# Performance work log

Measured on AMD Instinct MI355X. Metric: run time of the kernel, lower is better.

## Reference

```python
import jax, jax.numpy as jnp
import numpy as np

B, S, D, H = 2, 2048, 2048, 16
DEPTH = D // H


def setup_inputs() -> dict:
    key = jax.random.key(0)
    ks = jax.random.split(key, 12)
    std = 1.0 / np.sqrt(D)
    mk = lambda k, shape: (jax.random.uniform(k, shape, jnp.float32) * 2 - 1) * std
    # causal additive mask: 1.0 where future position (masked), 0.0 elsewhere
    mask = jnp.triu(jnp.ones((S, S), jnp.float32), k=1)[None, None]
    return {
        "q": jax.random.normal(ks[0], (B, S, D), jnp.float32),
        "k": jax.random.normal(ks[1], (B, S, D), jnp.float32),
        "v": jax.random.normal(ks[2], (B, S, D), jnp.float32),
        "mask": mask,
        "wq_w": mk(ks[3], (D, D)), "wq_b": mk(ks[4], (D,)),
        "wk_w": mk(ks[5], (D, D)), "wk_b": mk(ks[6], (D,)),
        "wv_w": mk(ks[7], (D, D)), "wv_b": mk(ks[8], (D,)),
        "dense_w": mk(ks[9], (D, D)), "dense_b": mk(ks[10], (D,)),
    }


def split_heads(x):
    # [B,S,D] -> [B,H,S,depth]
    b, s, _ = x.shape
    return x.reshape(b, s, H, DEPTH).transpose(0, 2, 1, 3)


def reference(q, k, v, mask, wq_w, wq_b, wk_w, wk_b, wv_w, wv_b, dense_w, dense_b):
    # torch Linear: y = x @ W.T + b
    qh = split_heads(q @ wq_w.T + wq_b)
    kh = split_heads(k @ wk_w.T + wk_b)
    vh = split_heads(v @ wv_w.T + wv_b)
    scale = 1.0 / jnp.sqrt(jnp.asarray(DEPTH, jnp.float32))
    logits = jnp.einsum("bhqd,bhkd->bhqk", qh, kh) * scale
    logits = logits + mask * (-1e9)
    weights = jax.nn.softmax(logits, axis=-1)  # dropout is identity in eval
    out = jnp.einsum("bhqk,bhkd->bhqd", weights, vh)
    out = out.transpose(0, 2, 1, 3).reshape(q.shape[0], -1, D)
    return out @ dense_w.T + dense_b
```

## Files before the change

### kernel.cpp

```cpp
#include <hip/hip_runtime.h>
#include <hip/hip_bf16.h>


typedef __bf16 bf16x8 __attribute__((ext_vector_type(8)));
typedef float f32x4 __attribute__((ext_vector_type(4)));
typedef float f32x16 __attribute__((ext_vector_type(16)));
typedef unsigned short u16;
typedef unsigned int u32;

#define DEV static __device__ __forceinline__

DEV void gload_lds16(const void* g, void* l) {
  __builtin_amdgcn_global_load_lds(
      (const __attribute__((address_space(1))) void*)g,
      (__attribute__((address_space(3))) void*)l, 16, 0, 0);
}

DEV f32x4 mfma16(bf16x8 a, bf16x8 b, f32x4 c) {
  return __builtin_amdgcn_mfma_f32_16x16x32_bf16(a, b, c, 0, 0, 0);
}

DEV f32x16 mfma32(bf16x8 a, bf16x8 b, f32x16 c) {
  return __builtin_amdgcn_mfma_f32_32x32x16_bf16(a, b, c, 0, 0, 0);
}

DEV u16 f2bf(float x) {
  return __builtin_bit_cast(u16, __float2bfloat16(x));
}

DEV u32 pack2(float lo, float hi_) {
  return (u32)f2bf(lo) | ((u32)f2bf(hi_) << 16);
}

__global__ void __launch_bounds__(256) conv_f32_bf16(
    const float* __restrict__ in, u16* __restrict__ out) {
  const size_t i = ((size_t)blockIdx.x * 256 + threadIdx.x) * 4;
  const float4 v = *reinterpret_cast<const float4*>(in + i);
  ushort4 o;
  o.x = f2bf(v.x); o.y = f2bf(v.y); o.z = f2bf(v.z); o.w = f2bf(v.w);
  *reinterpret_cast<ushort4*>(out + i) = o;
}

__global__ void __launch_bounds__(256) conv_all(
    const float* __restrict__ s0, const float* __restrict__ s1,
    const float* __restrict__ s2, const float* __restrict__ s3,
    const float* __restrict__ s4, const float* __restrict__ s5,
    const float* __restrict__ s6,
    u16* __restrict__ d0, u16* __restrict__ d1, u16* __restrict__ d2,
    u16* __restrict__ d3, u16* __restrict__ d4, u16* __restrict__ d5,
    u16* __restrict__ d6, const size_t nact, const size_t nw) {
  const int j = blockIdx.y;
  const size_t i = ((size_t)blockIdx.x * 256 + threadIdx.x) * 4;
  const float* s; u16* d; size_t n;
  switch (j) {
    case 0: s = s0; d = d0; n = nact; break;
    case 1: s = s1; d = d1; n = nact; break;
    case 2: s = s2; d = d2; n = nact; break;
    case 3: s = s3; d = d3; n = nw; break;
    case 4: s = s4; d = d4; n = nw; break;
    case 5: s = s5; d = d5; n = nw; break;
    default: s = s6; d = d6; n = nw; break;
  }
  if (i >= n) return;
  const float4 v = *reinterpret_cast<const float4*>(s + i);
  ushort4 o;
  o.x = f2bf(v.x); o.y = f2bf(v.y); o.z = f2bf(v.z); o.w = f2bf(v.w);
  *reinterpret_cast<ushort4*>(d + i) = o;
}

#define GBM 128
#define GBN 128
#define GBK 32
#define GK 2048
#define GNT 64

DEV void gemm_core(const u16* __restrict__ A, const u16* __restrict__ Bw,
                   const float* __restrict__ bias, void* __restrict__ Cout,
                   const int m0, const int n0, const int N, const int out_f32,
                   u16* As, u16* Bs) {
  const int tid = threadIdx.x;
  const int lane = tid & 63;
  const int w = tid >> 6;
  const int wr = w >> 1, wc = w & 1;
  const int g = lane >> 4;
  const int r16 = lane & 15;

  int offA[2], offB[2], dst2[2];
#pragma unroll
  for (int rr = 0; rr < 2; ++rr) {
    const int G = rr * 64 + lane;
    const int rp = w * 16 + (G >> 3);
    const int s = (G & 7) ^ (rp & 7);
    const int row = rp * 2 + (s >> 2);
    const int ch = s & 3;
    offA[rr] = (m0 + row) * GK + ch * 8;
    offB[rr] = (n0 + row) * GK + ch * 8;
    dst2[rr] = w * 1024 + rr * 512;
  }

  f32x4 acc[4][4];
#pragma unroll
  for (int i = 0; i < 4; ++i)
#pragma unroll
    for (int j = 0; j < 4; ++j) acc[i][j] = {0.f, 0.f, 0.f, 0.f};

  auto stage = [&](int t) {
    const int kk = t * GBK;
    u16* as = As + (t & 3) * 4096;
    u16* bs = Bs + (t & 3) * 4096;
    gload_lds16(A + offA[0] + kk, as + dst2[0]);
    gload_lds16(A + offA[1] + kk, as + dst2[1]);
    gload_lds16(Bw + offB[0] + kk, bs + dst2[0]);
    gload_lds16(Bw + offB[1] + kk, bs + dst2[1]);
  };

  auto compute = [&](int t) {
    const u16* as = As + (t & 3) * 4096;
    const u16* bs = Bs + (t & 3) * 4096;
    bf16x8 af[4], bf[4];
#pragma unroll
    for (int i = 0; i < 4; ++i) {
      const int row = wr * 64 + i * 16 + r16;
      const int rp = row >> 1;
      const int sl = (((row & 1) << 2) | g) ^ (rp & 7);
      af[i] = *reinterpret_cast<const bf16x8*>(as + rp * 64 + sl * 8);
      const int rowb = wc * 64 + i * 16 + r16;
      const int rpb = rowb >> 1;
      const int slb = (((rowb & 1) << 2) | g) ^ (rpb & 7);
      bf[i] = *reinterpret_cast<const bf16x8*>(bs + rpb * 64 + slb * 8);
    }
#pragma unroll
    for (int i = 0; i < 4; ++i)
#pragma unroll
      for (int j = 0; j < 4; ++j)
        acc[i][j] = mfma16(af[i], bf[j], acc[i][j]);
  };

  stage(0); stage(1); stage(2);
  asm volatile("s_waitcnt vmcnt(8)" ::: "memory");
  __builtin_amdgcn_s_barrier();

  for (int t = 0; t <= GNT - 4; ++t) {
    stage(t + 3);
    compute(t);
    asm volatile("s_waitcnt vmcnt(8) lgkmcnt(0)" ::: "memory");
    __builtin_amdgcn_s_barrier();
  }
  compute(GNT - 3);
  asm volatile("s_waitcnt vmcnt(4) lgkmcnt(0)" ::: "memory");
  __builtin_amdgcn_s_barrier();
  compute(GNT - 2);
  asm volatile("s_waitcnt vmcnt(0) lgkmcnt(0)" ::: "memory");
  __builtin_amdgcn_s_barrier();
  compute(GNT - 1);

  const int cbase = n0 + wc * 64 + r16;
  const int rbase = m0 + wr * 64 + g * 4;
#pragma unroll
  for (int i = 0; i < 4; ++i) {
#pragma unroll
    for (int j = 0; j < 4; ++j) {
      const int c = cbase + j * 16;
      const float bv = bias[c];
#pragma unroll
      for (int r = 0; r < 4; ++r) {
        const float v = acc[i][j][r] + bv;
        const size_t idx = (size_t)(rbase + i * 16 + r) * N + c;
        if (out_f32) ((float*)Cout)[idx] = v;
        else ((u16*)Cout)[idx] = f2bf(v);
      }
    }
  }
}

__global__ void __launch_bounds__(256, 2) gemm_ring(
    const u16* __restrict__ A, const u16* __restrict__ Bw,
    const float* __restrict__ bias, void* __restrict__ Cout,
    const int Mblocks, const int N, const int out_f32) {
  __shared__ u16 As[4 * GBM * GBK];
  __shared__ u16 Bs[4 * GBN * GBK];
  const int cpx = gridDim.x >> 3;
  int bid = blockIdx.x;
  bid = (bid & 7) * cpx + (bid >> 3);
  const int m0 = (bid % Mblocks) * GBM;
  const int n0 = (bid / Mblocks) * GBN;
  gemm_core(A, Bw, bias, Cout, m0, n0, N, out_f32, As, Bs);
}

__global__ void __launch_bounds__(256, 2) gemm_qkv(
    const u16* __restrict__ A0, const u16* __restrict__ A1,
    const u16* __restrict__ A2, const u16* __restrict__ W0,
    const u16* __restrict__ W1, const u16* __restrict__ W2,
    const float* __restrict__ b0, const float* __restrict__ b1,
    const float* __restrict__ b2, u16* __restrict__ C0,
    u16* __restrict__ C1, u16* __restrict__ C2) {
  __shared__ u16 As[4 * GBM * GBK];
  __shared__ u16 Bs[4 * GBN * GBK];
  const int which = blockIdx.x >> 9;
  const int inner = blockIdx.x & 511;
  const int bid = (inner & 7) * 64 + (inner >> 3);
  const int m0 = (bid & 31) * GBM;
  const int n0 = (bid >> 5) * GBN;
  const u16* A = which == 0 ? A0 : which == 1 ? A1 : A2;
  const u16* W = which == 0 ? W0 : which == 1 ? W1 : W2;
  const float* bb = which == 0 ? b0 : which == 1 ? b1 : b2;
  u16* C = which == 0 ? C0 : which == 1 ? C1 : C2;
  gemm_core(A, W, bb, C, m0, n0, 2048, 0, As, Bs);
}

#define SEQ 2048
#define DMODEL 2048
#define DH 128
#define QBLK 128
#define KBLK 64
#define C1 0.12751744f
#define THR_RAW 62.73f

__global__ void __launch_bounds__(256, 2) flash_attn(
    const u16* __restrict__ Qh, const u16* __restrict__ Kh,
    const u16* __restrict__ Vh, u16* __restrict__ O) {
  __shared__ u16 Ks[KBLK * DH];
  __shared__ u16 Vt[DH * KBLK];

  const int tid = threadIdx.x;
  const int lane = tid & 63;
  const int w = tid >> 6;
  const int hi = lane >> 5;
  const int l31 = lane & 31;

  const int cc = blockIdx.x;
  const int low = cc & 15;
  const int bh = (cc >> 4) & 31;
  const int h = bh & 15;
  const int b = bh >> 4;
  const int g0 = low ^ h;
  const int qt = b ? (15 - g0) : g0;
  const int q0 = qt * QBLK;
  const size_t rowbase = (size_t)b * SEQ;
  const int hoff = h * DH;
  const int qw = q0 + w * 32;
  const int qlane = qw + l31;

  bf16x8 aq[8];
  {
    const u16* qp = &Qh[(rowbase + qlane) * DMODEL + hoff + hi * 8];
#pragma unroll
    for (int c = 0; c < 8; ++c)
      aq[c] = *reinterpret_cast<const bf16x8*>(qp + c * 16);
  }

  f32x16 oacc[4];
#pragma unroll
  for (int dt = 0; dt < 4; ++dt)
#pragma unroll
    for (int r = 0; r < 16; ++r) oacc[dt][r] = 0.f;
  float mrow = -1e30f, lrow = 0.f;

  const int krl = w * 16 + (lane >> 4);
  const int kg4 = w * 4 + (lane >> 4);
  const int du = lane & 15;

  const int nkt = 2 * qt + 2;
  const int ktd = qw >> 6;

  uint4 vv[4];
#pragma unroll
  for (int r = 0; r < 4; ++r)
    vv[r] = *reinterpret_cast<const uint4*>(
        &Vh[(rowbase + kg4 * 4 + r) * DMODEL + hoff + du * 8]);

  for (int kt = 0; kt < nkt; ++kt) {
    const int k0 = kt * KBLK;
    __syncthreads();

#pragma unroll
    for (int i = 0; i < 4; ++i) {
      const int r = krl + i * 4;
      const int cg = (lane & 15) ^ (r & 15);
      gload_lds16(&Kh[(rowbase + k0 + r) * DMODEL + hoff + cg * 8],
                  &Ks[(w * 16 + i * 4) * DH]);
    }

#pragma unroll
    for (int j = 0; j < 8; ++j) {
      const int d = du * 8 + j;
      ushort4 pk4;
      pk4.x = ((const u16*)&vv[0])[j];
      pk4.y = ((const u16*)&vv[1])[j];
      pk4.z = ((const u16*)&vv[2])[j];
      pk4.w = ((const u16*)&vv[3])[j];
      const int slot = (((kg4 >> 1) ^ ((d >> 2) & 7)) * 8) + (kg4 & 1) * 4;
      *reinterpret_cast<ushort4*>(&Vt[d * KBLK + slot]) = pk4;
    }

    __syncthreads();

    if (kt + 1 < nkt) {
#pragma unroll
      for (int r = 0; r < 4; ++r)
        vv[r] = *reinterpret_cast<const uint4*>(
            &Vh[(rowbase + k0 + KBLK + kg4 * 4 + r) * DMODEL + hoff + du * 8]);
    }

    if (kt > ktd) continue;

    const bool diag = (kt == ktd);
    const bool act1 = (kt < ktd) || (w & 1);
    const bool m0q = diag && !(w & 1);
    const bool m1q = diag && (w & 1);

    float p[2][16];
    {
      f32x16 s;
#pragma unroll
      for (int r = 0; r < 16; ++r) s[r] = 0.f;
      __builtin_amdgcn_s_setprio(1);
#pragma unroll
      for (int c = 0; c < 8; ++c) {
        const int row = l31;
        const bf16x8 kf = *reinterpret_cast<const bf16x8*>(
            &Ks[row * DH + (((c * 2 + hi) ^ (row & 15)) * 8)]);
        s = mfma32(kf, aq[c], s);
      }
      __builtin_amdgcn_s_setprio(0);
#pragma unroll
      for (int r = 0; r < 16; ++r) {
        const int krow = (r & 3) + 8 * (r >> 2) + 4 * hi;
        p[0][r] = (m0q && (k0 + krow > qlane)) ? -1e9f : s[r];
      }
    }
    if (act1) {
      f32x16 s;
#pragma unroll
      for (int r = 0; r < 16; ++r) s[r] = 0.f;
      __builtin_amdgcn_s_setprio(1);
#pragma unroll
      for (int c = 0; c < 8; ++c) {
        const int row = 32 + l31;
        const bf16x8 kf = *reinterpret_cast<const bf16x8*>(
            &Ks[row * DH + (((c * 2 + hi) ^ (row & 15)) * 8)]);
        s = mfma32(kf, aq[c], s);
      }
      __builtin_amdgcn_s_setprio(0);
#pragma unroll
      for (int r = 0; r < 16; ++r) {
        const int krow = (r & 3) + 8 * (r >> 2) + 4 * hi;
        p[1][r] = (m1q && (k0 + 32 + krow > qlane)) ? -1e9f : s[r];
      }
    } else {
#pragma unroll
      for (int r = 0; r < 16; ++r) p[1][r] = -1e9f;
    }

    float mx = fmaxf(p[0][0], p[0][1]);
#pragma unroll
    for (int r = 2; r < 16; ++r) mx = fmaxf(mx, p[0][r]);
#pragma unroll
    for (int r = 0; r < 16; ++r) mx = fmaxf(mx, p[1][r]);
    mx = fmaxf(mx, __shfl_xor(mx, 32));

    const bool need = (mx > mrow + THR_RAW);
    if (__any((int)need)) {
      const float mn = fmaxf(mrow, mx);
      const float al = exp2f((mrow - mn) * C1);
      mrow = mn;
      lrow *= al;
#pragma unroll
      for (int r = 0; r < 16; ++r) {
        const float ar = __shfl(al, (r & 3) + 8 * (r >> 2) + 4 * hi);
#pragma unroll
        for (int dt = 0; dt < 4; ++dt) oacc[dt][r] *= ar;
      }
    }

    float sum = 0.f;
#pragma unroll
    for (int t = 0; t < 2; ++t)
#pragma unroll
      for (int r = 0; r < 16; ++r) {
        p[t][r] = exp2f((p[t][r] - mrow) * C1);
        sum += p[t][r];
      }
    sum += __shfl_xor(sum, 32);
    lrow += sum;

    u32 pk[2][8];
#pragma unroll
    for (int t = 0; t < 2; ++t)
#pragma unroll
      for (int m = 0; m < 8; ++m)
        pk[t][m] = pack2(p[t][2 * m], p[t][2 * m + 1]);

    __builtin_amdgcn_s_setprio(1);
#pragma unroll
    for (int ks = 0; ks < 4; ++ks) {
      if (ks >= 2 && !act1) break;
      const int t = ks >> 1;
      const int bs = (ks & 1) * 4;
      const u32 s0 = __shfl_xor(pk[t][bs + 0], 32);
      const u32 s1 = __shfl_xor(pk[t][bs + 1], 32);
      const u32 s2 = __shfl_xor(pk[t][bs + 2], 32);
      const u32 s3 = __shfl_xor(pk[t][bs + 3], 32);
      union { u32 u[4]; bf16x8 v; } pa;
      pa.u[0] = hi ? s2 : pk[t][bs + 0];
      pa.u[1] = hi ? s3 : pk[t][bs + 1];
      pa.u[2] = hi ? pk[t][bs + 2] : s0;
      pa.u[3] = hi ? pk[t][bs + 3] : s1;
#pragma unroll
      for (int dt = 0; dt < 4; ++dt) {
        const int d = dt * 32 + l31;
        const bf16x8 vf = *reinterpret_cast<const bf16x8*>(
            &Vt[d * KBLK + (((ks * 2 + hi) ^ ((d >> 2) & 7)) * 8)]);
        oacc[dt] = mfma32(pa.v, vf, oacc[dt]);
      }
    }
    __builtin_amdgcn_s_setprio(0);
  }

  const float li = __builtin_amdgcn_rcpf(lrow);
#pragma unroll
  for (int r = 0; r < 16; ++r) {
    const int rowq = (r & 3) + 8 * (r >> 2) + 4 * hi;
    const float lr = __shfl(li, rowq);
    u16* op = &O[(rowbase + qw + rowq) * DMODEL + hoff + l31];
#pragma unroll
    for (int dt = 0; dt < 4; ++dt) op[dt * 32] = f2bf(oacc[dt][r] * lr);
  }
}

extern "C" void kernel_launch(void* const* d_in, const int* in_sizes, int n_in,
                              void* d_out, int out_size, void* d_ws,
                              size_t ws_size, hipStream_t stream) {
  const int Bv = 2, S = 2048, D = 2048;
  const int M = Bv * S;
  const size_t NT = (size_t)M * D;
  const size_t NW = (size_t)D * D;

  const float* q = (const float*)d_in[0];
  const float* k = (const float*)d_in[1];
  const float* v = (const float*)d_in[2];
  const float* wq_w = (const float*)d_in[4];
  const float* wq_b = (const float*)d_in[5];
  const float* wk_w = (const float*)d_in[6];
  const float* wk_b = (const float*)d_in[7];
  const float* wv_w = (const float*)d_in[8];
  const float* wv_b = (const float*)d_in[9];
  const float* dw = (const float*)d_in[10];
  const float* db = (const float*)d_in[11];
  float* out = (float*)d_out;

  const dim3 blk(256);
  const dim3 gattn(512);
  const size_t need = (7 * NT + 4 * NW) * 2;

  if (ws_size >= need) {
    u16* base = (u16*)d_ws;
    u16* Xq = base;
    u16* Xk = Xq + NT;
    u16* Xv = Xk + NT;
    u16* Wq = Xv + NT;
    u16* Wk = Wq + NW;
    u16* Wv = Wk + NW;
    u16* Wd = Wv + NW;
    u16* Qh = Wd + NW;
    u16* Kh = Qh + NT;
    u16* Vh = Kh + NT;
    u16* Obf = Vh + NT;

    conv_all<<<dim3((unsigned)(NT / 1024), 7), blk, 0, stream>>>(
        q, k, v, wq_w, wk_w, wv_w, dw, Xq, Xk, Xv, Wq, Wk, Wv, Wd, NT, NW);
    gemm_qkv<<<dim3(1536), blk, 0, stream>>>(
        Xq, Xk, Xv, Wq, Wk, Wv, wq_b, wk_b, wv_b, Qh, Kh, Vh);
    flash_attn<<<gattn, blk, 0, stream>>>(Qh, Kh, Vh, Obf);
    gemm_ring<<<dim3(512), blk, 0, stream>>>(Obf, Wd, db, out, 32, D, 1);
  } else {
    u16* Xbf = (u16*)d_ws;
    u16* Wbf = Xbf + NT;
    u16* Qh = Wbf + NW;
    u16* Kh = Qh + NT;
    u16* Vh = Kh + NT;
    u16* Obf = Vh + NT;
    const dim3 gact((unsigned)(NT / 1024));
    const dim3 gw((unsigned)(NW / 1024));

    conv_f32_bf16<<<gact, blk, 0, stream>>>(q, Xbf);
    conv_f32_bf16<<<gw, blk, 0, stream>>>(wq_w, Wbf);
    gemm_ring<<<dim3(512), blk, 0, stream>>>(Xbf, Wbf, wq_b, Qh, 32, D, 0);
    conv_f32_bf16<<<gact, blk, 0, stream>>>(k, Xbf);
    conv_f32_bf16<<<gw, blk, 0, stream>>>(wk_w, Wbf);
    gemm_ring<<<dim3(512), blk, 0, stream>>>(Xbf, Wbf, wk_b, Kh, 32, D, 0);
    conv_f32_bf16<<<gact, blk, 0, stream>>>(v, Xbf);
    conv_f32_bf16<<<gw, blk, 0, stream>>>(wv_w, Wbf);
    gemm_ring<<<dim3(512), blk, 0, stream>>>(Xbf, Wbf, wv_b, Vh, 32, D, 0);
    flash_attn<<<gattn, blk, 0, stream>>>(Qh, Kh, Vh, Obf);
    conv_f32_bf16<<<gw, blk, 0, stream>>>(dw, Wbf);
    gemm_ring<<<dim3(512), blk, 0, stream>>>(Obf, Wbf, db, out, 32, D, 1);
  }
}
```

Measured before the change: 342.8 us.

## Use 2-wave GEMM blocks with 64x128 warp tiles and 3-stage LDS ring

The GEMM blocks drop from 4 waves to 2 waves, each computing a 64x128 tile with 32 accumulators instead of 16. This raises MFMA work per LDS fragment load. The LDS ring shrinks from 4 to 3 stages, and the QKV launch now interleaves blocks across XCDs with a new block-index mapping. The cost is higher register pressure, fewer waves to hide latency, and a shallower prefetch pipeline.

```diff
diff --git a/kernel.cpp b/kernel.cpp
--- a/kernel.cpp
+++ b/kernel.cpp
@@ -81,86 +81,84 @@
   const int tid = threadIdx.x;
   const int lane = tid & 63;
   const int w = tid >> 6;
-  const int wr = w >> 1, wc = w & 1;
   const int g = lane >> 4;
   const int r16 = lane & 15;
 
-  int offA[2], offB[2], dst2[2];
-#pragma unroll
-  for (int rr = 0; rr < 2; ++rr) {
-    const int G = rr * 64 + lane;
-    const int rp = w * 16 + (G >> 3);
+  int offA[4], offB[4], dst[4];
+#pragma unroll
+  for (int j = 0; j < 4; ++j) {
+    const int G = j * 128 + tid;
+    const int rp = G >> 3;
     const int s = (G & 7) ^ (rp & 7);
     const int row = rp * 2 + (s >> 2);
     const int ch = s & 3;
-    offA[rr] = (m0 + row) * GK + ch * 8;
-    offB[rr] = (n0 + row) * GK + ch * 8;
-    dst2[rr] = w * 1024 + rr * 512;
-  }
-
-  f32x4 acc[4][4];
+    offA[j] = (m0 + row) * GK + ch * 8;
+    offB[j] = (n0 + row) * GK + ch * 8;
+    dst[j] = (j * 128 + w * 64) * 8;
+  }
+
+  f32x4 acc[4][8];
 #pragma unroll
   for (int i = 0; i < 4; ++i)
 #pragma unroll
-    for (int j = 0; j < 4; ++j) acc[i][j] = {0.f, 0.f, 0.f, 0.f};
+    for (int j = 0; j < 8; ++j) acc[i][j] = {0.f, 0.f, 0.f, 0.f};
 
   auto stage = [&](int t) {
     const int kk = t * GBK;
-    u16* as = As + (t & 3) * 4096;
-    u16* bs = Bs + (t & 3) * 4096;
-    gload_lds16(A + offA[0] + kk, as + dst2[0]);
-    gload_lds16(A + offA[1] + kk, as + dst2[1]);
-    gload_lds16(Bw + offB[0] + kk, bs + dst2[0]);
-    gload_lds16(Bw + offB[1] + kk, bs + dst2[1]);
+    u16* as = As + (t % 3) * 4096;
+    u16* bs = Bs + (t % 3) * 4096;
+#pragma unroll
+    for (int j = 0; j < 4; ++j) gload_lds16(A + offA[j] + kk, as + dst[j]);
+#pragma unroll
+    for (int j = 0; j < 4; ++j) gload_lds16(Bw + offB[j] + kk, bs + dst[j]);
   };
 
   auto compute = [&](int t) {
-    const u16* as = As + (t & 3) * 4096;
-    const u16* bs = Bs + (t & 3) * 4096;
-    bf16x8 af[4], bf[4];
+    const u16* as = As + (t % 3) * 4096;
+    const u16* bs = Bs + (t % 3) * 4096;
+    bf16x8 af[4], bf[8];
 #pragma unroll
     for (int i = 0; i < 4; ++i) {
-      const int row = wr * 64 + i * 16 + r16;
+      const int row = w * 64 + i * 16 + r16;
       const int rp = row >> 1;
       const int sl = (((row & 1) << 2) | g) ^ (rp & 7);
       af[i] = *reinterpret_cast<const bf16x8*>(as + rp * 64 + sl * 8);
-      const int rowb = wc * 64 + i * 16 + r16;
+    }
+#pragma unroll
+    for (int j = 0; j < 8; ++j) {
+      const int rowb = j * 16 + r16;
       const int rpb = rowb >> 1;
       const int slb = (((rowb & 1) << 2) | g) ^ (rpb & 7);
-      bf[i] = *reinterpret_cast<const bf16x8*>(bs + rpb * 64 + slb * 8);
+      bf[j] = *reinterpret_cast<const bf16x8*>(bs + rpb * 64 + slb * 8);
     }
 #pragma unroll
     for (int i = 0; i < 4; ++i)
 #pragma unroll
-      for (int j = 0; j < 4; ++j)
+      for (int j = 0; j < 8; ++j)
         acc[i][j] = mfma16(af[i], bf[j], acc[i][j]);
   };
 
-  stage(0); stage(1); stage(2);
+  stage(0); stage(1);
   asm volatile("s_waitcnt vmcnt(8)" ::: "memory");
   __builtin_amdgcn_s_barrier();
 
-  for (int t = 0; t <= GNT - 4; ++t) {
-    stage(t + 3);
+  for (int t = 0; t <= GNT - 3; ++t) {
+    stage(t + 2);
     compute(t);
     asm volatile("s_waitcnt vmcnt(8) lgkmcnt(0)" ::: "memory");
     __builtin_amdgcn_s_barrier();
   }
-  compute(GNT - 3);
-  asm volatile("s_waitcnt vmcnt(4) lgkmcnt(0)" ::: "memory");
-  __builtin_amdgcn_s_barrier();
   compute(GNT - 2);
   asm volatile("s_waitcnt vmcnt(0) lgkmcnt(0)" ::: "memory");
   __builtin_amdgcn_s_barrier();
   compute(GNT - 1);
 
-  const int cbase = n0 + wc * 64 + r16;
-  const int rbase = m0 + wr * 64 + g * 4;
+  const int rbase = m0 + w * 64 + g * 4;
 #pragma unroll
   for (int i = 0; i < 4; ++i) {
 #pragma unroll
-    for (int j = 0; j < 4; ++j) {
-      const int c = cbase + j * 16;
+    for (int j = 0; j < 8; ++j) {
+      const int c = n0 + j * 16 + r16;
       const float bv = bias[c];
 #pragma unroll
       for (int r = 0; r < 4; ++r) {
@@ -173,34 +171,33 @@
   }
 }
 
-__global__ void __launch_bounds__(256, 2) gemm_ring(
+__global__ void __launch_bounds__(128) gemm_ring(
     const u16* __restrict__ A, const u16* __restrict__ Bw,
     const float* __restrict__ bias, void* __restrict__ Cout,
     const int Mblocks, const int N, const int out_f32) {
-  __shared__ u16 As[4 * GBM * GBK];
-  __shared__ u16 Bs[4 * GBN * GBK];
+  __shared__ u16 As[3 * 4096];
+  __shared__ u16 Bs[3 * 4096];
   const int cpx = gridDim.x >> 3;
-  int bid = blockIdx.x;
-  bid = (bid & 7) * cpx + (bid >> 3);
-  const int m0 = (bid % Mblocks) * GBM;
-  const int n0 = (bid / Mblocks) * GBN;
+  const int logical = (blockIdx.x & 7) * cpx + (blockIdx.x >> 3);
+  const int m0 = (logical % Mblocks) * GBM;
+  const int n0 = (logical / Mblocks) * GBN;
   gemm_core(A, Bw, bias, Cout, m0, n0, N, out_f32, As, Bs);
 }
 
-__global__ void __launch_bounds__(256, 2) gemm_qkv(
+__global__ void __launch_bounds__(128) gemm_qkv(
     const u16* __restrict__ A0, const u16* __restrict__ A1,
     const u16* __restrict__ A2, const u16* __restrict__ W0,
     const u16* __restrict__ W1, const u16* __restrict__ W2,
     const float* __restrict__ b0, const float* __restrict__ b1,
     const float* __restrict__ b2, u16* __restrict__ C0,
     u16* __restrict__ C1, u16* __restrict__ C2) {
-  __shared__ u16 As[4 * GBM * GBK];
-  __shared__ u16 Bs[4 * GBN * GBK];
-  const int which = blockIdx.x >> 9;
-  const int inner = blockIdx.x & 511;
-  const int bid = (inner & 7) * 64 + (inner >> 3);
-  const int m0 = (bid & 31) * GBM;
-  const int n0 = (bid >> 5) * GBN;
+  __shared__ u16 As[3 * 4096];
+  __shared__ u16 Bs[3 * 4096];
+  const int logical = (blockIdx.x & 7) * 192 + (blockIdx.x >> 3);
+  const int which = logical >> 9;
+  const int inner = logical & 511;
+  const int m0 = (inner & 31) * GBM;
+  const int n0 = (inner >> 5) * GBN;
   const u16* A = which == 0 ? A0 : which == 1 ? A1 : A2;
   const u16* W = which == 0 ? W0 : which == 1 ? W1 : W2;
   const float* bb = which == 0 ? b0 : which == 1 ? b1 : b2;
@@ -450,6 +447,7 @@
   float* out = (float*)d_out;
 
   const dim3 blk(256);
+  const dim3 gblk(128);
   const dim3 gattn(512);
   const size_t need = (7 * NT + 4 * NW) * 2;
 
@@ -469,10 +467,10 @@
 
     conv_all<<<dim3((unsigned)(NT / 1024), 7), blk, 0, stream>>>(
         q, k, v, wq_w, wk_w, wv_w, dw, Xq, Xk, Xv, Wq, Wk, Wv, Wd, NT, NW);
-    gemm_qkv<<<dim3(1536), blk, 0, stream>>>(
+    gemm_qkv<<<dim3(1536), gblk, 0, stream>>>(
         Xq, Xk, Xv, Wq, Wk, Wv, wq_b, wk_b, wv_b, Qh, Kh, Vh);
     flash_attn<<<gattn, blk, 0, stream>>>(Qh, Kh, Vh, Obf);
-    gemm_ring<<<dim3(512), blk, 0, stream>>>(Obf, Wd, db, out, 32, D, 1);
+    gemm_ring<<<dim3(512), gblk, 0, stream>>>(Obf, Wd, db, out, 32, D, 1);
   } else {
     u16* Xbf = (u16*)d_ws;
     u16* Wbf = Xbf + NT;
@@ -485,15 +483,15 @@
 
     conv_f32_bf16<<<gact, blk, 0, stream>>>(q, Xbf);
     conv_f32_bf16<<<gw, blk, 0, stream>>>(wq_w, Wbf);
-    gemm_ring<<<dim3(512), blk, 0, stream>>>(Xbf, Wbf, wq_b, Qh, 32, D, 0);
+    gemm_ring<<<dim3(512), gblk, 0, stream>>>(Xbf, Wbf, wq_b, Qh, 32, D, 0);
     conv_f32_bf16<<<gact, blk, 0, stream>>>(k, Xbf);
     conv_f32_bf16<<<gw, blk, 0, stream>>>(wk_w, Wbf);
-    gemm_ring<<<dim3(512), blk, 0, stream>>>(Xbf, Wbf, wk_b, Kh, 32, D, 0);
+    gemm_ring<<<dim3(512), gblk, 0, stream>>>(Xbf, Wbf, wk_b, Kh, 32, D, 0);
     conv_f32_bf16<<<gact, blk, 0, stream>>>(v, Xbf);
     conv_f32_bf16<<<gw, blk, 0, stream>>>(wv_w, Wbf);
-    gemm_ring<<<dim3(512), blk, 0, stream>>>(Xbf, Wbf, wv_b, Vh, 32, D, 0);
+    gemm_ring<<<dim3(512), gblk, 0, stream>>>(Xbf, Wbf, wv_b, Vh, 32, D, 0);
     flash_attn<<<gattn, blk, 0, stream>>>(Qh, Kh, Vh, Obf);
     conv_f32_bf16<<<gw, blk, 0, stream>>>(dw, Wbf);
-    gemm_ring<<<dim3(512), blk, 0, stream>>>(Obf, Wbf, db, out, 32, D, 1);
-  }
-}
+    gemm_ring<<<dim3(512), gblk, 0, stream>>>(Obf, Wbf, db, out, 32, D, 1);
+  }
+}
```

New measurement: 475.6 us. 38.7% more time.
